# Performance work log

Measured on AMD Instinct MI355X. Metric: run time of the kernel, lower is better.

The kernel has to match this reference:

```python
import jax, jax.numpy as jnp
import numpy as np

N = 100000      # nodes
E = 1600000     # edges (avg degree 16)
EMB = 64        # embedding_size (per-head out channels)
H = 2           # heads (hardcoded in module)
HID = 128       # hidden_size
NEG_SLOPE = 0.2 # GATv2 default


def setup_inputs() -> dict:
    key = jax.random.key(0)
    ks = jax.random.split(key, 12)
    s = 0.1
    x = jax.random.normal(ks[0], (N, 1), jnp.float32)
    edge_index = jax.random.randint(ks[1], (2, E), 0, N, dtype=jnp.int64)
    edge_attr = jax.random.normal(ks[2], (E, 1), jnp.float32)
    # GATv2Conv params (in_channels=1, out=EMB, heads=H, edge_dim=1)
    W_l = jax.random.normal(ks[3], (1, H * EMB), jnp.float32) * s
    b_l = jnp.zeros((H * EMB,), jnp.float32)
    W_r = jax.random.normal(ks[4], (1, H * EMB), jnp.float32) * s
    b_r = jnp.zeros((H * EMB,), jnp.float32)
    W_e = jax.random.normal(ks[5], (1, H * EMB), jnp.float32) * s   # lin_edge, bias=False
    att = jax.random.normal(ks[6], (H, EMB), jnp.float32) * s       # attention vector a
    bias_out = jnp.zeros((H * EMB,), jnp.float32)                   # conv output bias (concat=True)
    # fc: Linear(embedding_size*4, hidden_size)
    W_fc = jax.random.normal(ks[7], (HID, 4 * EMB), jnp.float32) * s
    b_fc = jnp.zeros((HID,), jnp.float32)
    return {
        "x": x, "edge_index": edge_index, "edge_attr": edge_attr,
        "target_node_idx": 123,
        "W_l": W_l, "b_l": b_l, "W_r": W_r, "b_r": b_r,
        "W_e": W_e, "att": att, "bias_out": bias_out,
        "W_fc": W_fc, "b_fc": b_fc,
    }


def reference(x, edge_index, edge_attr, target_node_idx,
              W_l, b_l, W_r, b_r, W_e, att, bias_out, W_fc, b_fc):
    n = x.shape[0]
    h, c = att.shape
    src, dst = edge_index[0], edge_index[1]

    # add_self_loops with fill_value='mean': per-target-node mean of incoming edge_attr
    deg = jax.ops.segment_sum(jnp.ones((src.shape[0],), x.dtype), dst, num_segments=n)
    attr_mean = jax.ops.segment_sum(edge_attr, dst, num_segments=n) / jnp.maximum(deg, 1.0)[:, None]
    loop = jnp.arange(n, dtype=src.dtype)
    src_f = jnp.concatenate([src, loop])
    dst_f = jnp.concatenate([dst, loop])
    ea = jnp.concatenate([edge_attr, attr_mean], axis=0)  # [E+N, 1]

    # per-head node transforms
    x_l = (x @ W_l + b_l).reshape(n, h, c)  # source transform
    x_r = (x @ W_r + b_r).reshape(n, h, c)  # target transform
    e_edge = (ea @ W_e).reshape(-1, h, c)   # edge-feature transform

    # GATv2: e_ij = a^T LeakyReLU(W_l x_j + W_r x_i + W_e e_ij)
    e = jax.nn.leaky_relu(x_l[src_f] + x_r[dst_f] + e_edge, NEG_SLOPE)  # [E', H, C]
    logits = jnp.einsum('ehc,hc->eh', e, att)  # [E', H]

    # segment softmax over incoming edges per target node
    m = jax.ops.segment_max(logits, dst_f, num_segments=n)     # [N, H]
    expv = jnp.exp(logits - m[dst_f])
    denom = jax.ops.segment_sum(expv, dst_f, num_segments=n)
    alpha = expv / denom[dst_f]                                 # [E', H]

    # weighted scatter-aggregate of source messages, concat heads, add bias
    out = jax.ops.segment_sum(alpha[:, :, None] * x_l[src_f], dst_f, num_segments=n)
    graph_emb = out.reshape(n, h * c) + bias_out                # [N, 2*EMB]

    # gather target, repeat, concat, linear
    tgt = graph_emb[target_node_idx]                            # [2*EMB]
    combined = jnp.concatenate([graph_emb, jnp.broadcast_to(tgt[None, :], graph_emb.shape)], axis=1)
    return combined @ W_fc.T + b_fc                             # [N, HID]
```

## Files before the change

### kernel.cpp

```cpp
#include <hip/hip_runtime.h>
#include <math.h>


#define LRELU_A1 0.6f
#define LRELU_A2 0.4f
#define TB       256
#define EPB      2048
#define NPB      128
#define NB_MAX   1024
#define SW       512

__global__ void k_prep(const unsigned int* __restrict__ ei,
                       const float* __restrict__ att,
                       const float* __restrict__ W_l,
                       const float* __restrict__ b_l, const float* __restrict__ b_r,
                       const float* __restrict__ bias_out,
                       const float* __restrict__ W_fc, const float* __restrict__ b_fc,
                       float* __restrict__ C) {
  int j = threadIdx.x;
  unsigned long long nz = __ballot(j < 32 && ei[2 * j + 1] != 0u);
  if (j == 0) ((int*)C)[1024] = (nz == 0ull) ? 1 : 0;
  if (j >= 128) return;
  float a = att[j];
  C[j] = LRELU_A1 * a;
  C[128 + j] = LRELU_A2 * a;
  C[256 + j] = b_l[j] + b_r[j];
  const float* wrow = W_fc + j * 256;
  float u0 = 0.f, u1 = 0.f, v0 = 0.f, v1 = 0.f, cb = b_fc[j];
  for (int c = 0; c < 64; c++) {
    u0 = fmaf(W_l[c],      wrow[c],       u0);
    u1 = fmaf(W_l[64 + c], wrow[64 + c],  u1);
    v0 = fmaf(W_l[c],      wrow[128 + c], v0);
    v1 = fmaf(W_l[64 + c], wrow[192 + c], v1);
  }
  for (int t = 0; t < 128; t++) {
    float gb = b_l[t] + bias_out[t];
    cb = fmaf(gb, wrow[t] + wrow[128 + t], cb);
  }
  C[384 + j] = u0;
  C[512 + j] = u1;
  C[640 + j] = v0;
  C[768 + j] = v1;
  C[896 + j] = cb;
}

#define CH_STEP(comp, ACC, i)                                                      \
  do {                                                                             \
    float v_ = fmaf(xs8[i], wl.comp, fmaf(xt8[i], wr.comp, fmaf(ae8[i], we.comp, bb.comp))); \
    ACC[i] = fmaf(a2.comp, fabsf(v_), fmaf(a1.comp, v_, ACC[i]));                  \
  } while (0)

__global__ __launch_bounds__(TB, 4) void k_bin(
    const float* __restrict__ x, const int* __restrict__ ei,
    const float* __restrict__ ea,
    const float* __restrict__ WL, const float* __restrict__ WR,
    const float* __restrict__ WE, const float* __restrict__ C,
    int4* __restrict__ rec, int* __restrict__ offsT,
    int NB, int S_BLOCKS, int E) {
  __shared__ int cnt[NB_MAX];
  __shared__ int pfx[NB_MAX + 1];
  __shared__ int sc[TB];
  const int tid = threadIdx.x;
  for (int i = tid; i < NB_MAX; i += TB) cnt[i] = 0;
  __syncthreads();

  const int e0 = blockIdx.x * EPB;
  const bool w64 = ((const int*)C)[1024] != 0;
  const float* A1 = C;
  const float* A2 = C + 128;
  const float* BASE = C + 256;

  int de8[8];
  float ae8[8], xs8[8], xt8[8];
  bool ok[8];
#pragma unroll
  for (int i = 0; i < 8; i++) {
    int e = e0 + i * TB + tid;
    ok[i] = (e < E);
    int ee = ok[i] ? e : 0;
    int s_ = w64 ? ei[2 * ee] : ei[ee];
    int d_ = w64 ? ei[2 * (E + ee)] : ei[E + ee];
    de8[i] = d_;
    ae8[i] = ea[ee];
    xs8[i] = x[s_];
    xt8[i] = x[d_];
  }
  float acc0[8] = {0.f, 0.f, 0.f, 0.f, 0.f, 0.f, 0.f, 0.f};
  float acc1[8] = {0.f, 0.f, 0.f, 0.f, 0.f, 0.f, 0.f, 0.f};
#pragma unroll 2
  for (int jb = 0; jb < 64; jb += 4) {
    float4 wl = *(const float4*)(WL + jb);
    float4 wr = *(const float4*)(WR + jb);
    float4 we = *(const float4*)(WE + jb);
    float4 bb = *(const float4*)(BASE + jb);
    float4 a1 = *(const float4*)(A1 + jb);
    float4 a2 = *(const float4*)(A2 + jb);
#pragma unroll
    for (int i = 0; i < 8; i++) {
      CH_STEP(x, acc0, i); CH_STEP(y, acc0, i); CH_STEP(z, acc0, i); CH_STEP(w, acc0, i);
    }
  }
#pragma unroll 2
  for (int jb = 64; jb < 128; jb += 4) {
    float4 wl = *(const float4*)(WL + jb);
    float4 wr = *(const float4*)(WR + jb);
    float4 we = *(const float4*)(WE + jb);
    float4 bb = *(const float4*)(BASE + jb);
    float4 a1 = *(const float4*)(A1 + jb);
    float4 a2 = *(const float4*)(A2 + jb);
#pragma unroll
    for (int i = 0; i < 8; i++) {
      CH_STEP(x, acc1, i); CH_STEP(y, acc1, i); CH_STEP(z, acc1, i); CH_STEP(w, acc1, i);
    }
  }
  int b8[8], slot8[8], p0[8], p1[8], p2[8], p3[8];
#pragma unroll
  for (int i = 0; i < 8; i++) {
    int d_ = de8[i];
    b8[i] = d_ >> 7;
    p0[i] = __float_as_int(__expf(acc0[i]));
    p1[i] = __float_as_int(__expf(acc1[i]));
    p2[i] = __float_as_int(xs8[i]);
    p3[i] = (int)((__float_as_uint(ae8[i]) & ~127u) | (unsigned)(d_ & 127));
    slot8[i] = ok[i] ? atomicAdd(&cnt[b8[i]], 1) : 0;
  }
  __syncthreads();
  int l4[4], mysum = 0;
#pragma unroll
  for (int j = 0; j < 4; j++) {
    int idx = tid * 4 + j;
    l4[j] = (idx < NB) ? cnt[idx] : 0;
    mysum += l4[j];
  }
  sc[tid] = mysum;
  __syncthreads();
  for (int st = 1; st < TB; st <<= 1) {
    int v = (tid >= st) ? sc[tid - st] : 0;
    __syncthreads();
    sc[tid] += v;
    __syncthreads();
  }
  int run = sc[tid] - mysum;
#pragma unroll
  for (int j = 0; j < 4; j++) {
    int idx = tid * 4 + j;
    if (idx < NB) { pfx[idx] = run; run += l4[j]; }
  }
  if (tid == 0) pfx[NB] = sc[TB - 1];
  __syncthreads();
  for (int b = tid; b <= NB; b += TB)
    offsT[(size_t)b * S_BLOCKS + blockIdx.x] = pfx[b];
  int4* myrec = rec + (size_t)blockIdx.x * EPB;
#pragma unroll
  for (int i = 0; i < 8; i++) {
    if (ok[i]) myrec[pfx[b8[i]] + slot8[i]] = make_int4(p0[i], p1[i], p2[i], p3[i]);
  }
}

__global__ __launch_bounds__(TB, 4) void k_reduce(
    const int4* __restrict__ rec, const int* __restrict__ offsT,
    float* __restrict__ Spart, int S_BLOCKS, int SPP) {
  __shared__ int4 sorted[SW];
  __shared__ int lut[SW];
  __shared__ int sc[TB];
  __shared__ int cnt[NPB];
  __shared__ int pos0[NPB];
  __shared__ int claim[NPB];
  const int tid = threadIdx.x;
  const int b = blockIdx.x;
  const int part = blockIdx.y;

  const int sA = part * SPP + tid;
  const int sB = sA + TB;
  int stA = 0, lenA = 0, stB = 0, lenB = 0;
  if (tid < SPP && sA < S_BLOCKS) {
    stA  = offsT[(size_t)b * S_BLOCKS + sA];
    lenA = offsT[(size_t)(b + 1) * S_BLOCKS + sA] - stA;
  }
  if (TB + tid < SPP && sB < S_BLOCKS) {
    stB  = offsT[(size_t)b * S_BLOCKS + sB];
    lenB = offsT[(size_t)(b + 1) * S_BLOCKS + sB] - stB;
  }
  const int rbA = sA * EPB + stA;
  const int rbB = sB * EPB + stB;
  const int mysum = lenA + lenB;
  sc[tid] = mysum;
  if (tid < NPB) cnt[tid] = 0;
  __syncthreads();
  for (int d = 1; d < TB; d <<= 1) {
    int v = (tid >= d) ? sc[tid - d] : 0;
    __syncthreads();
    sc[tid] += v;
    __syncthreads();
  }
  const int T = sc[TB - 1];
  const int bsA = sc[tid] - mysum;
  const int bsB = bsA + lenA;

  float r0 = 0.f, r1 = 0.f, r2 = 0.f, r3 = 0.f, r4 = 0.f;
  int rc = 0;

  for (int w0 = 0; w0 < T; w0 += SW) {
    const int w1 = min(w0 + SW, T);
    {
      int lo = max(bsA, w0), hi = min(bsA + lenA, w1);
      for (int k = lo; k < hi; k++) lut[k - w0] = rbA + (k - bsA);
      lo = max(bsB, w0); hi = min(bsB + lenB, w1);
      for (int k = lo; k < hi; k++) lut[k - w0] = rbB + (k - bsB);
    }
    __syncthreads();
    for (int i = w0 + tid; i < w1; i += TB) {
      int4 r = rec[(size_t)(unsigned)lut[i - w0]];
      atomicAdd(&cnt[(int)((unsigned)r.w & 127u)], 1);
    }
    __syncthreads();
    if (tid < 64) {
      int c0 = cnt[2 * tid], c1 = cnt[2 * tid + 1];
      int s = c0 + c1;
      for (int d = 1; d < 64; d <<= 1) {
        int t = __shfl_up(s, d);
        if (tid >= d) s += t;
      }
      int excl = s - (c0 + c1);
      pos0[2 * tid] = excl;
      pos0[2 * tid + 1] = excl + c0;
      claim[2 * tid] = excl;
      claim[2 * tid + 1] = excl + c0;
    }
    __syncthreads();
    for (int i = w0 + tid; i < w1; i += TB) {
      int4 r = rec[(size_t)(unsigned)lut[i - w0]];
      int node = (int)((unsigned)r.w & 127u);
      int slot = atomicAdd(&claim[node], 1);
      sorted[slot] = r;
    }
    __syncthreads();
    if (tid < NPB) {
      int p = pos0[tid], c = cnt[tid];
      for (int k = 0; k < c; k++) {
        int4 r = sorted[p + k];
        float e0v = __int_as_float(r.x);
        float e1v = __int_as_float(r.y);
        float xsv = __int_as_float(r.z);
        float aev = __uint_as_float((unsigned)r.w & ~127u);
        r0 += e0v;
        r1 += e0v * xsv;
        r2 += e1v;
        r3 += e1v * xsv;
        r4 += aev;
      }
      rc += c;
      cnt[tid] = 0;
    }
    __syncthreads();
  }
  if (tid < NPB) {
    float* out = Spart + ((size_t)b * gridDim.y + part) * (NPB * 6) + tid * 6;
    out[0] = r0; out[1] = r1; out[2] = r2;
    out[3] = r3; out[4] = r4; out[5] = (float)rc;
  }
}

__global__ __launch_bounds__(256) void k_fin(
    const float* __restrict__ x,
    const float* __restrict__ WL, const float* __restrict__ WR,
    const float* __restrict__ WE, const float* __restrict__ C,
    const float* __restrict__ Spart, float* __restrict__ S,
    int N, int P) {
  int n = blockIdx.x * blockDim.x + threadIdx.x;
  if (n >= N) return;
  int b = n >> 7, t = n & 127;
  const float* q0 = Spart + ((size_t)b * P) * (NPB * 6) + t * 6;
  float den0 = 0.f, num0 = 0.f, den1 = 0.f, num1 = 0.f, asum = 0.f, cntv = 0.f;
  for (int p = 0; p < P; p++) {
    const float* q = q0 + (size_t)p * (NPB * 6);
    float2 v0 = *(const float2*)(q);
    float2 v1 = *(const float2*)(q + 2);
    float2 v2 = *(const float2*)(q + 4);
    den0 += v0.x; num0 += v0.y;
    den1 += v1.x; num1 += v1.y;
    asum += v2.x; cntv += v2.y;
  }
  const float* A1 = C;
  const float* A2 = C + 128;
  const float* BASE = C + 256;
  float xn = x[n];
  float am = asum / fmaxf(cntv, 1.0f);
  float acc0 = 0.f, acc1 = 0.f;
#pragma unroll 4
  for (int jb = 0; jb < 64; jb += 4) {
    float4 wl = *(const float4*)(WL + jb);
    float4 wr = *(const float4*)(WR + jb);
    float4 we = *(const float4*)(WE + jb);
    float4 bb = *(const float4*)(BASE + jb);
    float4 a1 = *(const float4*)(A1 + jb);
    float4 a2 = *(const float4*)(A2 + jb);
    float v;
    v = fmaf(xn, wl.x + wr.x, fmaf(am, we.x, bb.x)); acc0 = fmaf(a2.x, fabsf(v), fmaf(a1.x, v, acc0));
    v = fmaf(xn, wl.y + wr.y, fmaf(am, we.y, bb.y)); acc0 = fmaf(a2.y, fabsf(v), fmaf(a1.y, v, acc0));
    v = fmaf(xn, wl.z + wr.z, fmaf(am, we.z, bb.z)); acc0 = fmaf(a2.z, fabsf(v), fmaf(a1.z, v, acc0));
    v = fmaf(xn, wl.w + wr.w, fmaf(am, we.w, bb.w)); acc0 = fmaf(a2.w, fabsf(v), fmaf(a1.w, v, acc0));
  }
#pragma unroll 4
  for (int jb = 64; jb < 128; jb += 4) {
    float4 wl = *(const float4*)(WL + jb);
    float4 wr = *(const float4*)(WR + jb);
    float4 we = *(const float4*)(WE + jb);
    float4 bb = *(const float4*)(BASE + jb);
    float4 a1 = *(const float4*)(A1 + jb);
    float4 a2 = *(const float4*)(A2 + jb);
    float v;
    v = fmaf(xn, wl.x + wr.x, fmaf(am, we.x, bb.x)); acc1 = fmaf(a2.x, fabsf(v), fmaf(a1.x, v, acc1));
    v = fmaf(xn, wl.y + wr.y, fmaf(am, we.y, bb.y)); acc1 = fmaf(a2.y, fabsf(v), fmaf(a1.y, v, acc1));
    v = fmaf(xn, wl.z + wr.z, fmaf(am, we.z, bb.z)); acc1 = fmaf(a2.z, fabsf(v), fmaf(a1.z, v, acc1));
    v = fmaf(xn, wl.w + wr.w, fmaf(am, we.w, bb.w)); acc1 = fmaf(a2.w, fabsf(v), fmaf(a1.w, v, acc1));
  }
  float s0 = __expf(acc0), s1 = __expf(acc1);
  float2 sv;
  sv.x = (num0 + s0 * xn) / (den0 + s0);
  sv.y = (num1 + s1 * xn) / (den1 + s1);
  *(float2*)(S + 2 * n) = sv;
}

__global__ __launch_bounds__(256) void k_out(
    const float* __restrict__ S, const float* __restrict__ C,
    const int* __restrict__ tgtp, float* __restrict__ out, int N) {
  int g = blockIdx.x * blockDim.x + threadIdx.x;
  if (g >= N * 32) return;
  int n = g >> 5;
  int kq = (g & 31) * 4;
  int T = tgtp[0];
  float s0t = S[2 * T], s1t = S[2 * T + 1];
  float2 s = *(const float2*)(S + 2 * n);
  float4 u0 = *(const float4*)(C + 384 + kq);
  float4 u1 = *(const float4*)(C + 512 + kq);
  float4 v0 = *(const float4*)(C + 640 + kq);
  float4 v1 = *(const float4*)(C + 768 + kq);
  float4 cb = *(const float4*)(C + 896 + kq);
  float4 o;
  o.x = fmaf(s.x, u0.x, fmaf(s.y, u1.x, fmaf(s0t, v0.x, fmaf(s1t, v1.x, cb.x))));
  o.y = fmaf(s.x, u0.y, fmaf(s.y, u1.y, fmaf(s0t, v0.y, fmaf(s1t, v1.y, cb.y))));
  o.z = fmaf(s.x, u0.z, fmaf(s.y, u1.z, fmaf(s0t, v0.z, fmaf(s1t, v1.z, cb.z))));
  o.w = fmaf(s.x, u0.w, fmaf(s.y, u1.w, fmaf(s0t, v0.w, fmaf(s1t, v1.w, cb.w))));
  *(float4*)(out + n * 128 + kq) = o;
}

extern "C" void kernel_launch(void* const* d_in, const int* in_sizes, int n_in,
                              void* d_out, int out_size, void* d_ws, size_t ws_size,
                              hipStream_t stream) {
  const float* x        = (const float*)d_in[0];
  const int*   ei       = (const int*)d_in[1];
  const float* ea       = (const float*)d_in[2];
  const int*   tgt      = (const int*)d_in[3];
  const float* W_l      = (const float*)d_in[4];
  const float* b_l      = (const float*)d_in[5];
  const float* W_r      = (const float*)d_in[6];
  const float* b_r      = (const float*)d_in[7];
  const float* W_e      = (const float*)d_in[8];
  const float* att      = (const float*)d_in[9];
  const float* bias_out = (const float*)d_in[10];
  const float* W_fc     = (const float*)d_in[11];
  const float* b_fc     = (const float*)d_in[12];

  const int N = in_sizes[0];
  const int E = in_sizes[2];
  const int NB = (N + NPB - 1) / NPB;
  const int S_BLOCKS = (E + EPB - 1) / EPB;

  const size_t sz_rec  = (size_t)S_BLOCKS * EPB * 16;
  const size_t sz_offs = (size_t)(NB + 1) * S_BLOCKS * 4;
  const size_t sz_S    = (size_t)2 * N * 4;
  const size_t sz_C    = 4608;
  int P = 8;
  while (P > 2 &&
         sz_rec + sz_offs + sz_S + sz_C + (size_t)NB * P * NPB * 6 * 4 > ws_size)
    P >>= 1;
  const int SPP = (S_BLOCKS + P - 1) / P;

  char* p = (char*)d_ws;
  int4*  rec   = (int4*)p;                      p += sz_rec;
  int*   offsT = (int*)p;                       p += sz_offs;
  float* S     = (float*)p;                     p += sz_S;
  float* C     = (float*)p;                     p += sz_C;
  float* Spart = (float*)p;

  k_prep<<<1, 128, 0, stream>>>((const unsigned int*)ei, att, W_l, b_l, b_r,
                                bias_out, W_fc, b_fc, C);
  k_bin<<<S_BLOCKS, TB, 0, stream>>>(x, ei, ea, W_l, W_r, W_e, C,
                                     rec, offsT, NB, S_BLOCKS, E);
  k_reduce<<<dim3(NB, P), TB, 0, stream>>>(rec, offsT, Spart, S_BLOCKS, SPP);
  k_fin<<<(N + 255) / 256, 256, 0, stream>>>(x, W_l, W_r, W_e, C, Spart, S, N, P);
  k_out<<<(N * 32 + 255) / 256, 256, 0, stream>>>(S, C, tgt, (float*)d_out, N);
}
```

Before: 207.5 us.

## Halve edges per bin block and use wavefront shuffle scans

Lowers edges per binning block from 2048 to 1024, which doubles the number of bin blocks and lowers register pressure in k_bin. Both k_bin and k_reduce now do their block-wide prefix scans with 64-lane __shfl_up scans plus a small per-wave sum array, replacing the shared-memory Hillis-Steele scan that needed many __syncthreads. The aim is fewer barriers and more parallelism in binning. The cost is that S_BLOCKS doubles, so the offsets table and the number of segments k_reduce must gather both grow.

```diff
diff --git a/kernel.cpp b/kernel.cpp
--- a/kernel.cpp
+++ b/kernel.cpp
@@ -5,7 +5,8 @@
 #define LRELU_A1 0.6f
 #define LRELU_A2 0.4f
 #define TB       256
-#define EPB      2048
+#define EPB      1024
+#define NE       (EPB / TB)
 #define NPB      128
 #define NB_MAX   1024
 #define SW       512
@@ -59,7 +60,7 @@
     int NB, int S_BLOCKS, int E) {
   __shared__ int cnt[NB_MAX];
   __shared__ int pfx[NB_MAX + 1];
-  __shared__ int sc[TB];
+  __shared__ int wsum[4];
   const int tid = threadIdx.x;
   for (int i = tid; i < NB_MAX; i += TB) cnt[i] = 0;
   __syncthreads();
@@ -70,11 +71,11 @@
   const float* A2 = C + 128;
   const float* BASE = C + 256;
 
-  int de8[8];
-  float ae8[8], xs8[8], xt8[8];
-  bool ok[8];
-#pragma unroll
-  for (int i = 0; i < 8; i++) {
+  int de8[NE];
+  float ae8[NE], xs8[NE], xt8[NE];
+  bool ok[NE];
+#pragma unroll
+  for (int i = 0; i < NE; i++) {
     int e = e0 + i * TB + tid;
     ok[i] = (e < E);
     int ee = ok[i] ? e : 0;
@@ -85,8 +86,9 @@
     xs8[i] = x[s_];
     xt8[i] = x[d_];
   }
-  float acc0[8] = {0.f, 0.f, 0.f, 0.f, 0.f, 0.f, 0.f, 0.f};
-  float acc1[8] = {0.f, 0.f, 0.f, 0.f, 0.f, 0.f, 0.f, 0.f};
+  float acc0[NE], acc1[NE];
+#pragma unroll
+  for (int i = 0; i < NE; i++) { acc0[i] = 0.f; acc1[i] = 0.f; }
 #pragma unroll 2
   for (int jb = 0; jb < 64; jb += 4) {
     float4 wl = *(const float4*)(WL + jb);
@@ -96,7 +98,7 @@
     float4 a1 = *(const float4*)(A1 + jb);
     float4 a2 = *(const float4*)(A2 + jb);
 #pragma unroll
-    for (int i = 0; i < 8; i++) {
+    for (int i = 0; i < NE; i++) {
       CH_STEP(x, acc0, i); CH_STEP(y, acc0, i); CH_STEP(z, acc0, i); CH_STEP(w, acc0, i);
     }
   }
@@ -109,13 +111,13 @@
     float4 a1 = *(const float4*)(A1 + jb);
     float4 a2 = *(const float4*)(A2 + jb);
 #pragma unroll
-    for (int i = 0; i < 8; i++) {
+    for (int i = 0; i < NE; i++) {
       CH_STEP(x, acc1, i); CH_STEP(y, acc1, i); CH_STEP(z, acc1, i); CH_STEP(w, acc1, i);
     }
   }
-  int b8[8], slot8[8], p0[8], p1[8], p2[8], p3[8];
-#pragma unroll
-  for (int i = 0; i < 8; i++) {
+  int b8[NE], slot8[NE], p0[NE], p1[NE], p2[NE], p3[NE];
+#pragma unroll
+  for (int i = 0; i < NE; i++) {
     int d_ = de8[i];
     b8[i] = d_ >> 7;
     p0[i] = __float_as_int(__expf(acc0[i]));
@@ -132,27 +134,31 @@
     l4[j] = (idx < NB) ? cnt[idx] : 0;
     mysum += l4[j];
   }
-  sc[tid] = mysum;
+  const int lane = tid & 63, wv = tid >> 6;
+  int inc = mysum;
+#pragma unroll
+  for (int d = 1; d < 64; d <<= 1) {
+    int t = __shfl_up(inc, d);
+    if (lane >= d) inc += t;
+  }
+  if (lane == 63) wsum[wv] = inc;
   __syncthreads();
-  for (int st = 1; st < TB; st <<= 1) {
-    int v = (tid >= st) ? sc[tid - st] : 0;
-    __syncthreads();
-    sc[tid] += v;
-    __syncthreads();
-  }
-  int run = sc[tid] - mysum;
+  int wbase = 0;
+#pragma unroll
+  for (int w = 0; w < 4; w++) if (w < wv) wbase += wsum[w];
+  int run = wbase + inc - mysum;
 #pragma unroll
   for (int j = 0; j < 4; j++) {
     int idx = tid * 4 + j;
     if (idx < NB) { pfx[idx] = run; run += l4[j]; }
   }
-  if (tid == 0) pfx[NB] = sc[TB - 1];
+  if (tid == 0) pfx[NB] = wsum[0] + wsum[1] + wsum[2] + wsum[3];
   __syncthreads();
   for (int b = tid; b <= NB; b += TB)
     offsT[(size_t)b * S_BLOCKS + blockIdx.x] = pfx[b];
   int4* myrec = rec + (size_t)blockIdx.x * EPB;
 #pragma unroll
-  for (int i = 0; i < 8; i++) {
+  for (int i = 0; i < NE; i++) {
     if (ok[i]) myrec[pfx[b8[i]] + slot8[i]] = make_int4(p0[i], p1[i], p2[i], p3[i]);
   }
 }
@@ -162,10 +168,10 @@
     float* __restrict__ Spart, int S_BLOCKS, int SPP) {
   __shared__ int4 sorted[SW];
   __shared__ int lut[SW];
-  __shared__ int sc[TB];
   __shared__ int cnt[NPB];
   __shared__ int pos0[NPB];
   __shared__ int claim[NPB];
+  __shared__ int wsum[4];
   const int tid = threadIdx.x;
   const int b = blockIdx.x;
   const int part = blockIdx.y;
@@ -184,17 +190,21 @@
   const int rbA = sA * EPB + stA;
   const int rbB = sB * EPB + stB;
   const int mysum = lenA + lenB;
-  sc[tid] = mysum;
   if (tid < NPB) cnt[tid] = 0;
+  const int lane = tid & 63, wv = tid >> 6;
+  int inc = mysum;
+#pragma unroll
+  for (int d = 1; d < 64; d <<= 1) {
+    int t = __shfl_up(inc, d);
+    if (lane >= d) inc += t;
+  }
+  if (lane == 63) wsum[wv] = inc;
   __syncthreads();
-  for (int d = 1; d < TB; d <<= 1) {
-    int v = (tid >= d) ? sc[tid - d] : 0;
-    __syncthreads();
-    sc[tid] += v;
-    __syncthreads();
-  }
-  const int T = sc[TB - 1];
-  const int bsA = sc[tid] - mysum;
+  int wbase = 0;
+#pragma unroll
+  for (int w = 0; w < 4; w++) if (w < wv) wbase += wsum[w];
+  const int T = wsum[0] + wsum[1] + wsum[2] + wsum[3];
+  const int bsA = wbase + inc - mysum;
   const int bsB = bsA + lenA;
 
   float r0 = 0.f, r1 = 0.f, r2 = 0.f, r3 = 0.f, r4 = 0.f;
```

Result: no change. 206.3 us (-0.5%).
